# Optimization experiments

Measured on AMD Instinct MI355X. Metric: run time of the kernel, lower is better.

## Reference

```python
import jax, jax.numpy as jnp
import numpy as np

BLOCK = 64  # block_size from config
NEG_INF = -1e9


def setup_inputs() -> dict:
    key = jax.random.key(0)
    k1, k2, k3, k4 = jax.random.split(key, 4)
    B, H, S, D = 2, 8, 2048, 64
    nb = S // BLOCK  # 32 blocks per side
    query = jax.random.normal(k1, (B, H, S, D), dtype=jnp.float32)
    key_t = jax.random.normal(k2, (B, H, S, D), dtype=jnp.float32)
    value = jax.random.normal(k3, (B, H, S, D), dtype=jnp.float32)
    # binary block mask; force diagonal blocks on so every row has >=1 valid key
    mat = jax.random.randint(k4, (nb, nb), 0, 2).astype(jnp.int32)
    mat = mat.at[jnp.arange(nb), jnp.arange(nb)].set(1)
    mask = jnp.ones((B, S), dtype=jnp.float32)  # padding mask (1 = keep)
    return {"query": query, "key": key_t, "value": value, "mask": mask, "mat": mat}


def reference(query, key, value, mask, mat):
    # Upsample block mask [nb, nb] -> dense [S, S] (nearest, like nn.Upsample)
    block_dense = jnp.repeat(jnp.repeat(mat, BLOCK, axis=0), BLOCK, axis=1) > 0
    # Block-sparse QK^T: only positions inside nonzero blocks participate.
    scores = jnp.einsum('bhqd,bhkd->bhqk', query, key)
    # Additive padding-mask bias, as in the original: 1e6 * (1 - mask)
    scores = scores - 1e6 * (1.0 - mask)[:, None, None, :]
    # Positions outside the block pattern are excluded from the softmax.
    scores = jnp.where(block_dense[None, None, :, :], scores, NEG_INF)
    attn = jax.nn.softmax(scores, axis=-1)
    out = jnp.einsum('bhqk,bhkd->bhqd', attn, value)
    return out
```

## Files before the change

kernel.cpp:

```cpp
#include <hip/hip_runtime.h>


typedef __attribute__((ext_vector_type(8))) short short8;
typedef __attribute__((ext_vector_type(4))) short short4_;
typedef __attribute__((ext_vector_type(4))) float float4_;
typedef __attribute__((ext_vector_type(8))) _Float16 half8_;

#define B_   2
#define H_   8
#define S_   2048
#define D_   64
#define NB_  32
#define KP   72
#define LOG2E 1.4426950408889634f

__device__ __forceinline__ short f2bf(float f) {
    union { float f; unsigned int u; } x; x.f = f;
    unsigned int r = x.u + 0x7FFFu + ((x.u >> 16) & 1u);
    return (short)(r >> 16);
}
__device__ __forceinline__ short f2bf_t(float f) {
    union { float f; unsigned int u; } x; x.f = f;
    return (short)(x.u >> 16);
}
__device__ __forceinline__ float bf2f(short s) {
    union { unsigned int u; float f; } x; x.u = ((unsigned int)(unsigned short)s) << 16;
    return x.f;
}
__device__ __forceinline__ short f2h(float f) {
    _Float16 h = (_Float16)f;
    return __builtin_bit_cast(short, h);
}
__device__ __forceinline__ int swz(int row, int gran) {
    return (row << 6) + (((gran ^ row) & 7) << 3);
}
__device__ __forceinline__ void gload16(const short* g, short* l) {
    __builtin_amdgcn_global_load_lds(
        (const __attribute__((address_space(1))) void*)g,
        (__attribute__((address_space(3))) void*)l, 16, 0, 0);
}

__global__ __launch_bounds__(256)
void preconvert_kernel(const float* __restrict__ K, const float* __restrict__ V,
                       short* __restrict__ Khf, short* __restrict__ Vtb) {
    const int tid = threadIdx.x;
    const int kt  = blockIdx.x;
    const int bh  = blockIdx.y;
    const size_t src = ((size_t)bh * S_ + kt * 64) * D_;
    const size_t dst = ((size_t)(bh * NB_ + kt)) << 12;

#pragma unroll
    for (int it = 0; it < 4; ++it) {
        int i = tid + it * 256;
        int row = i >> 4, c4 = (i & 15) * 4;
        float4_ kv = *(const float4_*)(K + src + row * D_ + c4);
        short4_ kh;
#pragma unroll
        for (int e = 0; e < 4; ++e) kh[e] = f2h(kv[e] * LOG2E);
        *(short4_*)(Khf + dst + swz(row, c4 >> 3) + (c4 & 7)) = kh;
    }

    {
        const int key4 = (tid >> 4) << 2;
        const int d4   = (tid & 15) << 2;
        const float* vp = V + src + (size_t)key4 * D_ + d4;
        float4_ r0 = *(const float4_*)(vp);
        float4_ r1 = *(const float4_*)(vp + D_);
        float4_ r2 = *(const float4_*)(vp + 2 * D_);
        float4_ r3 = *(const float4_*)(vp + 3 * D_);
#pragma unroll
        for (int cc = 0; cc < 4; ++cc) {
            short4_ col;
            col[0] = f2bf(r0[cc]); col[1] = f2bf(r1[cc]);
            col[2] = f2bf(r2[cc]); col[3] = f2bf(r3[cc]);
            int d = d4 + cc;
            *(short4_*)(Vtb + dst + swz(d, key4 >> 3) + (key4 & 7)) = col;
        }
    }
}

__global__ __launch_bounds__(512, 4)
void attn_fused(const float* __restrict__ Q,
                const float* __restrict__ Msk,
                const int* __restrict__ Mat,
                float* __restrict__ O,
                const short* __restrict__ Khf_g,
                const short* __restrict__ Vtb_g) {
    __shared__ __align__(16) short lds[40960];

    const int tid  = threadIdx.x;
    const int wave = tid >> 6;
    const int half = wave >> 2;
    const int w4   = wave & 3;
    const int lane = tid & 63;
    const int c    = lane & 15;
    const int quad = lane >> 4;

    const int qb = blockIdx.x;
    const int bh = blockIdx.y;
    const int b  = bh / H_;
    const size_t base = (size_t)bh * S_ * D_;

    unsigned long long bmv = __ballot(Mat[qb * NB_ + (lane & 31)] != 0);
    unsigned int mb = (unsigned int)(bmv & 0xFFFFFFFFull);
    const int nact  = __popc(mb);
    const int niter = (nact + 1) >> 1;
    unsigned int mine = 0;
    {
        unsigned int tb2 = mb; int idx = 0;
        while (tb2) {
            int k = __builtin_ctz(tb2); tb2 &= tb2 - 1;
            if ((idx & 1) == half) mine |= (1u << k);
            ++idx;
        }
    }

    int kb; bool kill;
    if (mine) { kb = __builtin_ctz(mine); mine &= mine - 1; kill = false; }
    else      { kb = __builtin_ctz(mb); kill = true; }
    {
        const size_t tb = ((size_t)(bh * NB_ + kb)) << 12;
        const int kd = (half << 12) + (w4 << 10);
        const short* gk = Khf_g + tb + (w4 << 10) + lane * 8;
        const short* gv = Vtb_g + tb + (w4 << 10) + lane * 8;
        gload16(gk,       &lds[kd]);
        gload16(gk + 512, &lds[kd + 512]);
        gload16(gv,       &lds[16384 + kd]);
        gload16(gv + 512, &lds[16384 + kd + 512]);
    }

    float biasc[4], biasn[4] = {0.f, 0.f, 0.f, 0.f};
#pragma unroll
    for (int t = 0; t < 4; ++t)
        biasc[t] = kill ? -2.0e6f
                        : -1.0e6f * LOG2E * (1.0f - Msk[(size_t)b * S_ + kb * 64 + t * 16 + c]);

    half8_ qa0, qa1;
    {
        const float* qp = Q + base + (size_t)(qb * 64 + w4 * 16 + c) * D_ + quad * 8;
        float4_ q0 = *(const float4_*)(qp);
        float4_ q1 = *(const float4_*)(qp + 4);
        float4_ q2 = *(const float4_*)(qp + 32);
        float4_ q3 = *(const float4_*)(qp + 36);
#pragma unroll
        for (int e = 0; e < 4; ++e) {
            qa0[e]     = (_Float16)q0[e];
            qa0[e + 4] = (_Float16)q1[e];
            qa1[e]     = (_Float16)q2[e];
            qa1[e + 4] = (_Float16)q3[e];
        }
    }

    float4_ o[4];
    float l_part[4];
#pragma unroll
    for (int t = 0; t < 4; ++t) { o[t][0] = 0.f; o[t][1] = 0.f; o[t][2] = 0.f; o[t][3] = 0.f; }
#pragma unroll
    for (int j = 0; j < 4; ++j) l_part[j] = 0.f;

    int foff_lo[4], foff_hi[4];
#pragma unroll
    for (int t = 0; t < 4; ++t) {
        foff_lo[t] = swz(t * 16 + c, quad);
        foff_hi[t] = swz(t * 16 + c, quad + 4);
    }
    const int pwoff = 32768 + (wave << 10);
    const int prd0  = pwoff + swz(c, quad);
    const int prd1  = pwoff + swz(c, quad + 4);

    int cur = 0;
    for (int it2 = 0; it2 < niter; ++it2) {
        bool nkill = true;
        if (it2 + 1 < niter && mine) { kb = __builtin_ctz(mine); mine &= mine - 1; nkill = false; }

        __syncthreads();

        if (it2 + 1 < niter) {
            const size_t tb = ((size_t)(bh * NB_ + kb)) << 12;
            const int kd = ((cur ^ 1) << 13) + (half << 12) + (w4 << 10);
            const short* gk = Khf_g + tb + (w4 << 10) + lane * 8;
            const short* gv = Vtb_g + tb + (w4 << 10) + lane * 8;
            gload16(gk,       &lds[kd]);
            gload16(gk + 512, &lds[kd + 512]);
            gload16(gv,       &lds[16384 + kd]);
            gload16(gv + 512, &lds[16384 + kd + 512]);
#pragma unroll
            for (int t = 0; t < 4; ++t)
                biasn[t] = nkill ? -2.0e6f
                                 : -1.0e6f * LOG2E * (1.0f - Msk[(size_t)b * S_ + kb * 64 + t * 16 + c]);
        }

        const int kbase = (cur << 13) + (half << 12);
        const int vbase = 16384 + kbase;

        float4_ sc[4];
#pragma unroll
        for (int t = 0; t < 4; ++t) { sc[t][0] = 0.f; sc[t][1] = 0.f; sc[t][2] = 0.f; sc[t][3] = 0.f; }
        __builtin_amdgcn_s_setprio(1);
#pragma unroll
        for (int t = 0; t < 4; ++t) {
            half8_ kf0 = __builtin_bit_cast(half8_, *(const short8*)&lds[kbase + foff_lo[t]]);
            half8_ kf1 = __builtin_bit_cast(half8_, *(const short8*)&lds[kbase + foff_hi[t]]);
            sc[t] = __builtin_amdgcn_mfma_f32_16x16x32_f16(qa0, kf0, sc[t], 0, 0, 0);
            sc[t] = __builtin_amdgcn_mfma_f32_16x16x32_f16(qa1, kf1, sc[t], 0, 0, 0);
        }
        __builtin_amdgcn_s_setprio(0);

#pragma unroll
        for (int t = 0; t < 4; ++t) {
            const int cg = (t << 1) + (c >> 3);
#pragma unroll
            for (int j = 0; j < 4; ++j) {
                float p = __builtin_amdgcn_exp2f(sc[t][j] + biasc[t]);
                l_part[j] += p;
                const int row = quad * 4 + j;
                lds[pwoff + (row << 6) + (((cg ^ row) & 7) << 3) + (c & 7)] = f2bf_t(p);
            }
        }

        short8 pa0 = *(const short8*)&lds[prd0];
        short8 pa1 = *(const short8*)&lds[prd1];

        __builtin_amdgcn_s_setprio(1);
#pragma unroll
        for (int t = 0; t < 4; ++t) {
            short8 vb0 = *(const short8*)&lds[vbase + foff_lo[t]];
            short8 vb1 = *(const short8*)&lds[vbase + foff_hi[t]];
            o[t] = __builtin_amdgcn_mfma_f32_16x16x32_bf16(pa0, vb0, o[t], 0, 0, 0);
            o[t] = __builtin_amdgcn_mfma_f32_16x16x32_bf16(pa1, vb1, o[t], 0, 0, 0);
        }
        __builtin_amdgcn_s_setprio(0);

#pragma unroll
        for (int t = 0; t < 4; ++t) biasc[t] = biasn[t];
        cur ^= 1;
    }

    __syncthreads();
    float* fl = (float*)lds;
    if (half == 1) {
        const int idx = ((wave - 4) * 64 + lane) * 21;
#pragma unroll
        for (int t = 0; t < 4; ++t)
#pragma unroll
            for (int j = 0; j < 4; ++j) fl[idx + t * 4 + j] = o[t][j];
#pragma unroll
        for (int j = 0; j < 4; ++j) fl[idx + 16 + j] = l_part[j];
    }
    __syncthreads();
    if (half == 0) {
        const int idx = (wave * 64 + lane) * 21;
#pragma unroll
        for (int j = 0; j < 4; ++j) {
            float rs = l_part[j] + fl[idx + 16 + j];
            rs += __shfl_xor(rs, 1);
            rs += __shfl_xor(rs, 2);
            rs += __shfl_xor(rs, 4);
            rs += __shfl_xor(rs, 8);
            float inv = 1.0f / rs;
            size_t rowoff = base + (size_t)(qb * 64 + w4 * 16 + quad * 4 + j) * D_;
#pragma unroll
            for (int t = 0; t < 4; ++t)
                O[rowoff + t * 16 + c] = (o[t][j] + fl[idx + t * 4 + j]) * inv;
        }
    }
}

__global__ __launch_bounds__(256, 2)
void attn_mfma_fb(const float* __restrict__ Q,
                  const float* __restrict__ K,
                  const float* __restrict__ V,
                  const float* __restrict__ Msk,
                  const int* __restrict__ Mat,
                  float* __restrict__ O) {
    __shared__ __align__(16) short lds[4 * 64 * KP];
    short* Khi = lds;
    short* Klo = lds + 64 * KP;
    short* Vt  = lds + 2 * 64 * KP;
    short* Pl  = lds + 3 * 64 * KP;

    const int tid  = threadIdx.x;
    const int wave = tid >> 6;
    const int lane = tid & 63;
    const int c    = lane & 15;
    const int quad = lane >> 4;

    const int qb = blockIdx.x;
    const int bh = blockIdx.y;
    const int b  = bh / H_;
    const size_t base = (size_t)bh * S_ * D_;

    short8 qh0, qh1, ql0, ql1;
    {
        const float* qp = Q + base + (size_t)(qb * 64 + wave * 16 + c) * D_ + quad * 8;
#pragma unroll
        for (int e = 0; e < 8; ++e) {
            float f0 = qp[e], f1 = qp[e + 32];
            qh0[e] = f2bf(f0); ql0[e] = f2bf(f0 - bf2f(qh0[e]));
            qh1[e] = f2bf(f1); ql1[e] = f2bf(f1 - bf2f(qh1[e]));
        }
    }

    float4_ o[4];
    float l_part[4];
#pragma unroll
    for (int t = 0; t < 4; ++t) { o[t][0] = 0.f; o[t][1] = 0.f; o[t][2] = 0.f; o[t][3] = 0.f; }
#pragma unroll
    for (int j = 0; j < 4; ++j) l_part[j] = 0.f;

    for (int kb = 0; kb < NB_; ++kb) {
        if (Mat[qb * NB_ + kb] == 0) continue;

        __syncthreads();
        {
            const float* kg = K + base + (size_t)kb * 64 * D_;
            const float* vg = V + base + (size_t)kb * 64 * D_;
#pragma unroll
            for (int it = 0; it < 4; ++it) {
                int i = tid + it * 256;
                int row = i >> 4, c4 = (i & 15) * 4;
                float4_ kv = *(const float4_*)(kg + row * D_ + c4);
                short4_ hi, lo;
#pragma unroll
                for (int e = 0; e < 4; ++e) {
                    hi[e] = f2bf(kv[e]);
                    lo[e] = f2bf(kv[e] - bf2f(hi[e]));
                }
                *(short4_*)&Khi[row * KP + c4] = hi;
                *(short4_*)&Klo[row * KP + c4] = lo;
                float4_ vv = *(const float4_*)(vg + row * D_ + c4);
#pragma unroll
                for (int e = 0; e < 4; ++e) Vt[(c4 + e) * KP + row] = f2bf(vv[e]);
            }
        }
        __syncthreads();

        float4_ sc[4];
#pragma unroll
        for (int t = 0; t < 4; ++t) { sc[t][0] = 0.f; sc[t][1] = 0.f; sc[t][2] = 0.f; sc[t][3] = 0.f; }
#pragma unroll
        for (int t = 0; t < 4; ++t) {
            const short* kph = &Khi[(t * 16 + c) * KP + quad * 8];
            const short* kpl = &Klo[(t * 16 + c) * KP + quad * 8];
            short8 kh0 = *(const short8*)(kph);
            short8 kh1 = *(const short8*)(kph + 32);
            short8 kl0 = *(const short8*)(kpl);
            short8 kl1 = *(const short8*)(kpl + 32);
            sc[t] = __builtin_amdgcn_mfma_f32_16x16x32_bf16(qh0, kh0, sc[t], 0, 0, 0);
            sc[t] = __builtin_amdgcn_mfma_f32_16x16x32_bf16(qh1, kh1, sc[t], 0, 0, 0);
            sc[t] = __builtin_amdgcn_mfma_f32_16x16x32_bf16(qh0, kl0, sc[t], 0, 0, 0);
            sc[t] = __builtin_amdgcn_mfma_f32_16x16x32_bf16(qh1, kl1, sc[t], 0, 0, 0);
            sc[t] = __builtin_amdgcn_mfma_f32_16x16x32_bf16(ql0, kh0, sc[t], 0, 0, 0);
            sc[t] = __builtin_amdgcn_mfma_f32_16x16x32_bf16(ql1, kh1, sc[t], 0, 0, 0);
        }

        short* Pw = Pl + wave * 16 * KP;
#pragma unroll
        for (int t = 0; t < 4; ++t) {
            float bias = -1.0e6f * (1.0f - Msk[(size_t)b * S_ + kb * 64 + t * 16 + c]);
#pragma unroll
            for (int j = 0; j < 4; ++j) {
                float p = __expf(sc[t][j] + bias);
                l_part[j] += p;
                Pw[(quad * 4 + j) * KP + t * 16 + c] = f2bf(p);
            }
        }

        const short* pp = Pl + wave * 16 * KP + c * KP + quad * 8;
        short8 pa0 = *(const short8*)(pp);
        short8 pa1 = *(const short8*)(pp + 32);

#pragma unroll
        for (int t = 0; t < 4; ++t) {
            const short* vp = &Vt[(t * 16 + c) * KP + quad * 8];
            short8 vb0 = *(const short8*)(vp);
            short8 vb1 = *(const short8*)(vp + 32);
            o[t] = __builtin_amdgcn_mfma_f32_16x16x32_bf16(pa0, vb0, o[t], 0, 0, 0);
            o[t] = __builtin_amdgcn_mfma_f32_16x16x32_bf16(pa1, vb1, o[t], 0, 0, 0);
        }
    }

#pragma unroll
    for (int j = 0; j < 4; ++j) {
        float rs = l_part[j];
        rs += __shfl_xor(rs, 1);
        rs += __shfl_xor(rs, 2);
        rs += __shfl_xor(rs, 4);
        rs += __shfl_xor(rs, 8);
        float inv = 1.0f / rs;
        size_t rowoff = base + (size_t)(qb * 64 + wave * 16 + quad * 4 + j) * D_;
#pragma unroll
        for (int t = 0; t < 4; ++t)
            O[rowoff + t * 16 + c] = o[t][j] * inv;
    }
}

extern "C" void kernel_launch(void* const* d_in, const int* in_sizes, int n_in,
                              void* d_out, int out_size, void* d_ws, size_t ws_size,
                              hipStream_t stream) {
    const float* q   = (const float*)d_in[0];
    const float* k   = (const float*)d_in[1];
    const float* v   = (const float*)d_in[2];
    const float* msk = (const float*)d_in[3];
    const int*   mat = (const int*)d_in[4];
    float*       out = (float*)d_out;

    const size_t elems = (size_t)B_ * H_ * S_ * D_;
    const size_t need  = 2 * elems * sizeof(short);
    const int use_pre  = (ws_size >= need) ? 1 : 0;

    short* khf = (short*)d_ws;
    short* vtb = khf + elems;

    if (use_pre) {
        dim3 pgrid(NB_, B_ * H_);
        preconvert_kernel<<<pgrid, dim3(256), 0, stream>>>(k, v, khf, vtb);
        dim3 grid(NB_, B_ * H_);
        attn_fused<<<grid, dim3(512), 0, stream>>>(q, msk, mat, out, khf, vtb);
    } else {
        dim3 grid(NB_, B_ * H_);
        attn_mfma_fb<<<grid, dim3(256), 0, stream>>>(q, k, v, msk, mat, out);
    }
}
```

Baseline: 105.2 us.

## Remap workgroups to XCDs per head and transpose V through LDS

Both kernels now use a 1D grid whose block index is remapped, so that all query/key tiles of the same batch-head land on the same XCD. The aim is for K/V preconverted data to be reused in that XCD's L2 instead of spread across all eight. The preconvert kernel also changes its V transpose: rows are staged into padded LDS and then written out as 16-byte bf16 columns, replacing scattered 8-byte writes. The cost is an extra LDS round trip and a barrier, plus a dependence on round-robin XCD dispatch for the L2 locality to hold.

```diff
diff --git a/kernel.cpp b/kernel.cpp
--- a/kernel.cpp
+++ b/kernel.cpp
@@ -12,6 +12,7 @@
 #define D_   64
 #define NB_  32
 #define KP   72
+#define KP2  66
 #define LOG2E 1.4426950408889634f
 
 __device__ __forceinline__ short f2bf(float f) {
@@ -39,13 +40,20 @@
         (const __attribute__((address_space(1))) void*)g,
         (__attribute__((address_space(3))) void*)l, 16, 0, 0);
 }
+__device__ __forceinline__ void wg_remap(int n, int& bh, int& idx) {
+    const int xcd = n & 7;
+    const int sub = n >> 3;
+    bh  = (xcd << 1) + (sub & 1);
+    idx = sub >> 1;
+}
 
 __global__ __launch_bounds__(256)
 void preconvert_kernel(const float* __restrict__ K, const float* __restrict__ V,
                        short* __restrict__ Khf, short* __restrict__ Vtb) {
+    __shared__ short vn[64 * KP2];
     const int tid = threadIdx.x;
-    const int kt  = blockIdx.x;
-    const int bh  = blockIdx.y;
+    int bh, kt;
+    wg_remap(blockIdx.x, bh, kt);
     const size_t src = ((size_t)bh * S_ + kt * 64) * D_;
     const size_t dst = ((size_t)(bh * NB_ + kt)) << 12;
 
@@ -58,24 +66,22 @@
 #pragma unroll
         for (int e = 0; e < 4; ++e) kh[e] = f2h(kv[e] * LOG2E);
         *(short4_*)(Khf + dst + swz(row, c4 >> 3) + (c4 & 7)) = kh;
-    }
-
-    {
-        const int key4 = (tid >> 4) << 2;
-        const int d4   = (tid & 15) << 2;
-        const float* vp = V + src + (size_t)key4 * D_ + d4;
-        float4_ r0 = *(const float4_*)(vp);
-        float4_ r1 = *(const float4_*)(vp + D_);
-        float4_ r2 = *(const float4_*)(vp + 2 * D_);
-        float4_ r3 = *(const float4_*)(vp + 3 * D_);
-#pragma unroll
-        for (int cc = 0; cc < 4; ++cc) {
-            short4_ col;
-            col[0] = f2bf(r0[cc]); col[1] = f2bf(r1[cc]);
-            col[2] = f2bf(r2[cc]); col[3] = f2bf(r3[cc]);
-            int d = d4 + cc;
-            *(short4_*)(Vtb + dst + swz(d, key4 >> 3) + (key4 & 7)) = col;
-        }
+        float4_ vv = *(const float4_*)(V + src + row * D_ + c4);
+        short4_ vb;
+#pragma unroll
+        for (int e = 0; e < 4; ++e) vb[e] = f2bf(vv[e]);
+        *(short4_*)&vn[row * KP2 + c4] = vb;
+    }
+    __syncthreads();
+
+#pragma unroll
+    for (int it = 0; it < 2; ++it) {
+        int i = tid + it * 256;
+        int d = i >> 3, g = i & 7;
+        short8 o;
+#pragma unroll
+        for (int e = 0; e < 8; ++e) o[e] = vn[(g * 8 + e) * KP2 + d];
+        *(short8*)(Vtb + dst + swz(d, g)) = o;
     }
 }
 
@@ -96,8 +102,8 @@
     const int c    = lane & 15;
     const int quad = lane >> 4;
 
-    const int qb = blockIdx.x;
-    const int bh = blockIdx.y;
+    int bh, qb;
+    wg_remap(blockIdx.x, bh, qb);
     const int b  = bh / H_;
     const size_t base = (size_t)bh * S_ * D_;
 
@@ -413,10 +419,8 @@
     short* vtb = khf + elems;
 
     if (use_pre) {
-        dim3 pgrid(NB_, B_ * H_);
-        preconvert_kernel<<<pgrid, dim3(256), 0, stream>>>(k, v, khf, vtb);
-        dim3 grid(NB_, B_ * H_);
-        attn_fused<<<grid, dim3(512), 0, stream>>>(q, msk, mat, out, khf, vtb);
+        preconvert_kernel<<<dim3(NB_ * B_ * H_), dim3(256), 0, stream>>>(k, v, khf, vtb);
+        attn_fused<<<dim3(NB_ * B_ * H_), dim3(512), 0, stream>>>(q, msk, mat, out, khf, vtb);
     } else {
         dim3 grid(NB_, B_ * H_);
         attn_mfma_fb<<<grid, dim3(256), 0, stream>>>(q, k, v, msk, mat, out);
```

Measured after the change: 104.7 us. No clear change (-0.5%).
